# Kernel tuning notes

Measured on AMD Instinct MI355X. Metric: run time of the kernel, lower is better.

## Reference

```python
import jax, jax.numpy as jnp
import numpy as np

LORA_ALPHA = 16.0
TOP_K = 2


def setup_inputs() -> dict:
    key = jax.random.key(0)
    k_x, k_w, k_g, k_a, k_b = jax.random.split(key, 5)
    B, S, H, O, E, R = 2, 2048, 2048, 2048, 8, 16
    x = jax.random.normal(k_x, (B, S, H), dtype=jnp.float32)
    weight = jax.random.normal(k_w, (O, H), dtype=jnp.float32)          # frozen base W [out, in]
    gate_w = jax.random.normal(k_g, (E, H), dtype=jnp.float32) * 0.02   # router gate [E, in]
    A_w = jax.random.normal(k_a, (E, R, H), dtype=jnp.float32) * (1.0 / np.sqrt(H))  # stacked lora_A
    B_w = jax.random.normal(k_b, (E, O, R), dtype=jnp.float32) * 0.01   # stacked lora_B
    return {"x": x, "weight": weight, "gate_w": gate_w, "A_w": A_w, "B_w": B_w}


def reference(x, weight, gate_w, A_w, B_w):
    E = gate_w.shape[0]
    # Base frozen linear: F.linear(x, weight)
    out = jnp.einsum("bsh,oh->bso", x, weight)

    # Router: softmax over experts, top-2, renormalize
    logits = jnp.einsum("bsh,eh->bse", x, gate_w)
    probs = jax.nn.softmax(logits, axis=-1)
    topk_w, topk_idx = jax.lax.top_k(probs, TOP_K)          # [b,s,2]
    topk_w = topk_w / jnp.sum(topk_w, axis=-1, keepdims=True)

    # Per-token combine weight for each expert (sum over the 2 slots)
    onehot = jax.nn.one_hot(topk_idx, E, dtype=x.dtype)      # [b,s,2,E]
    cw = jnp.einsum("bsk,bske->bse", topk_w, onehot)         # [b,s,E]

    # LoRA: down-project into all experts' rank spaces, weight, then up-project.
    # t: [b,s,E,r] is small (r=16); weighting here avoids a [b,s,E,out] buffer.
    t = jnp.einsum("bsh,erh->bser", x, A_w)
    t = t * cw[..., None]
    lora = jnp.einsum("bser,eor->bso", t, B_w)

    return out + LORA_ALPHA * lora
```

## Files before the change

### kernel.cpp

```cpp
#include <hip/hip_runtime.h>
#include <hip/hip_bf16.h>


typedef __bf16 bf16x8 __attribute__((ext_vector_type(8)));
typedef float f32x4 __attribute__((ext_vector_type(4)));

__device__ __forceinline__ __bf16 f2bf(float f) {
  union { float f; unsigned u; } v; v.f = f;
  unsigned r = (v.u + 0x7FFFu + ((v.u >> 16) & 1u)) >> 16;
  unsigned short s = (unsigned short)r;
  return __builtin_bit_cast(__bf16, s);
}

__device__ __forceinline__ void ld_lds16(const void* g, void* l) {
  __builtin_amdgcn_global_load_lds((__attribute__((address_space(1))) void*)g,
                                   (__attribute__((address_space(3))) void*)l,
                                   16, 0, 0);
}

__global__ void conv2048(const float* __restrict__ src, __bf16* __restrict__ dst,
                         int dld) {
  const size_t r = blockIdx.x;
  const int c = threadIdx.x * 8;
  const float4* s = (const float4*)(src + r * 2048 + c);
  float4 a = s[0], b = s[1];
  bf16x8 v;
  v[0] = f2bf(a.x); v[1] = f2bf(a.y); v[2] = f2bf(a.z); v[3] = f2bf(a.w);
  v[4] = f2bf(b.x); v[5] = f2bf(b.y); v[6] = f2bf(b.z); v[7] = f2bf(b.w);
  *(bf16x8*)(dst + r * dld + c) = v;
}

__global__ void pack_bw(const float* __restrict__ Bw, __bf16* __restrict__ Bfull) {
  const int idx = blockIdx.x * 256 + threadIdx.x;
  const int e = idx >> 11, o = idx & 2047;
  const float4* s = (const float4*)(Bw + ((size_t)e * 2048 + o) * 16);
  float4 v0 = s[0], v1 = s[1], v2 = s[2], v3 = s[3];
  __bf16* d = Bfull + (size_t)o * 2176 + 2048 + e * 16;
  bf16x8 lo, hi;
  lo[0] = f2bf(v0.x); lo[1] = f2bf(v0.y); lo[2] = f2bf(v0.z); lo[3] = f2bf(v0.w);
  lo[4] = f2bf(v1.x); lo[5] = f2bf(v1.y); lo[6] = f2bf(v1.z); lo[7] = f2bf(v1.w);
  hi[0] = f2bf(v2.x); hi[1] = f2bf(v2.y); hi[2] = f2bf(v2.z); hi[3] = f2bf(v2.w);
  hi[4] = f2bf(v3.x); hi[5] = f2bf(v3.y); hi[6] = f2bf(v3.z); hi[7] = f2bf(v3.w);
  *(bf16x8*)d = lo;
  *(bf16x8*)(d + 8) = hi;
}

__global__ void router_kernel(const float* __restrict__ x, const float* __restrict__ gw,
                              __bf16* __restrict__ Abuf, float* __restrict__ cw) {
  const int t = blockIdx.x, tid = threadIdx.x;
  const float* xr = x + (size_t)t * 2048;
  const int c = tid * 8;
  float4 v0 = *(const float4*)(xr + c);
  float4 v1 = *(const float4*)(xr + c + 4);
  float xs[8] = {v0.x, v0.y, v0.z, v0.w, v1.x, v1.y, v1.z, v1.w};
  bf16x8 bv;
#pragma unroll
  for (int j = 0; j < 8; ++j) bv[j] = f2bf(xs[j]);
  *(bf16x8*)(Abuf + (size_t)t * 2176 + c) = bv;

  float acc[8] = {0, 0, 0, 0, 0, 0, 0, 0};
#pragma unroll
  for (int j = 0; j < 8; ++j) {
    const float xv = xs[j];
#pragma unroll
    for (int e = 0; e < 8; ++e) acc[e] += xv * gw[e * 2048 + c + j];
  }
#pragma unroll
  for (int e = 0; e < 8; ++e)
    for (int off = 32; off; off >>= 1) acc[e] += __shfl_down(acc[e], off);

  __shared__ float red[4][8];
  const int wave = tid >> 6, lane = tid & 63;
  if (lane == 0) {
#pragma unroll
    for (int e = 0; e < 8; ++e) red[wave][e] = acc[e];
  }
  __syncthreads();
  if (tid == 0) {
    float lg[8];
#pragma unroll
    for (int e = 0; e < 8; ++e) lg[e] = red[0][e] + red[1][e] + red[2][e] + red[3][e];
    int a = 0;
    for (int e = 1; e < 8; ++e) if (lg[e] > lg[a]) a = e;
    int b = (a == 0) ? 1 : 0;
    for (int e = 0; e < 8; ++e) if (e != a && lg[e] > lg[b]) b = e;
    const float d = __expf(lg[b] - lg[a]);
    const float wa = 1.0f / (1.0f + d), wb = d / (1.0f + d);
    float o[8] = {0, 0, 0, 0, 0, 0, 0, 0};
    o[a] = wa; o[b] = wb;
#pragma unroll
    for (int e = 0; e < 8; ++e) cw[t * 8 + e] = o[e];
  }
}

__global__ void t2_finish(const float* __restrict__ tpart, const float* __restrict__ cw,
                          __bf16* __restrict__ Abuf) {
  const int idx = blockIdx.x * 256 + threadIdx.x;
  const int t = idx >> 7, k2 = idx & 127;
  float s = tpart[idx] + tpart[idx + 524288] + tpart[idx + 2 * 524288] +
            tpart[idx + 3 * 524288];
  const float w = cw[t * 8 + (k2 >> 4)] * 16.0f;
  Abuf[(size_t)t * 2176 + 2048 + k2] = f2bf(s * w);
}

__global__ __launch_bounds__(256) void mfma_gemm_bt(
    const __bf16* __restrict__ A, const __bf16* __restrict__ B,
    float* __restrict__ C, int lda, int ldb, int ldc, int kiters,
    long long czstride) {
  __shared__ __align__(16) __bf16 As[128 * 64];
  __shared__ __align__(16) __bf16 Bs[128 * 64];
  const int tid = threadIdx.x;
  const int wave = tid >> 6;
  const int lane = tid & 63;
  const int tm = blockIdx.x * 128;
  const int tn = blockIdx.y * 128;
  C += (long long)blockIdx.z * czstride;

  const int wm = (wave >> 1) * 64;
  const int wn = (wave & 1) * 64;
  const int srow = lane >> 3;
  const int skoff = (lane & 7) * 8;

  f32x4 acc[4][4] = {};

  int kcur = blockIdx.z * kiters * 64;
  for (int kt = 0; kt < kiters; ++kt) {
#pragma unroll
    for (int r = 0; r < 4; ++r) {
      const int ch = r * 4 + wave;
      ld_lds16(A + (size_t)(tm + ch * 8 + srow) * lda + kcur + skoff, &As[ch * 512]);
      ld_lds16(B + (size_t)(tn + ch * 8 + srow) * ldb + kcur + skoff, &Bs[ch * 512]);
    }
    __syncthreads();
#pragma unroll
    for (int ks = 0; ks < 2; ++ks) {
      bf16x8 af[4], bfg[4];
#pragma unroll
      for (int i = 0; i < 4; ++i)
        af[i] = *(const bf16x8*)&As[(wm + i * 16 + (lane & 15)) * 64 + ks * 32 + (lane >> 4) * 8];
#pragma unroll
      for (int j = 0; j < 4; ++j)
        bfg[j] = *(const bf16x8*)&Bs[(wn + j * 16 + (lane & 15)) * 64 + ks * 32 + (lane >> 4) * 8];
#pragma unroll
      for (int i = 0; i < 4; ++i)
#pragma unroll
        for (int j = 0; j < 4; ++j)
          acc[i][j] = __builtin_amdgcn_mfma_f32_16x16x32_bf16(af[i], bfg[j], acc[i][j], 0, 0, 0);
    }
    __syncthreads();
    kcur += 64;
  }

  const int crow0 = tm + wm + (lane >> 4) * 4;
  const int ccol0 = tn + wn + (lane & 15);
#pragma unroll
  for (int i = 0; i < 4; ++i)
#pragma unroll
    for (int j = 0; j < 4; ++j)
#pragma unroll
      for (int rg = 0; rg < 4; ++rg)
        C[(size_t)(crow0 + i * 16 + rg) * ldc + ccol0 + j * 16] = acc[i][j][rg];
}

extern "C" void kernel_launch(void* const* d_in, const int* in_sizes, int n_in,
                              void* d_out, int out_size, void* d_ws, size_t ws_size,
                              hipStream_t stream) {
  const float* x = (const float*)d_in[0];
  const float* weight = (const float*)d_in[1];
  const float* gate_w = (const float*)d_in[2];
  const float* A_w = (const float*)d_in[3];
  const float* B_w = (const float*)d_in[4];
  float* out = (float*)d_out;

  char* ws = (char*)d_ws;
  __bf16* Abuf = (__bf16*)ws;
  __bf16* Bfull = (__bf16*)(ws + 17825792);
  __bf16* A2 = (__bf16*)(ws + 26738688);
  float* tpart = (float*)(ws + 27262976);
  float* cw = (float*)(ws + 35651584);

  conv2048<<<2048, 256, 0, stream>>>(weight, Bfull, 2176);
  conv2048<<<128, 256, 0, stream>>>(A_w, A2, 2048);
  pack_bw<<<64, 256, 0, stream>>>(B_w, Bfull);
  router_kernel<<<4096, 256, 0, stream>>>(x, gate_w, Abuf, cw);
  mfma_gemm_bt<<<dim3(32, 1, 4), 256, 0, stream>>>(Abuf, A2, tpart, 2176, 2048, 128,
                                                   8, 524288LL);
  t2_finish<<<2048, 256, 0, stream>>>(tpart, cw, Abuf);
  mfma_gemm_bt<<<dim3(32, 16, 1), 256, 0, stream>>>(Abuf, Bfull, out, 2176, 2176,
                                                    2048, 34, 0LL);
}
```

Baseline: 189.9 us.

## Swizzle GEMM LDS layout, merge prep kernels, stage gate weights in LDS

```diff
diff --git a/kernel.cpp b/kernel.cpp
--- a/kernel.cpp
+++ b/kernel.cpp
@@ -18,68 +18,83 @@
                                    16, 0, 0);
 }
 
-__global__ void conv2048(const float* __restrict__ src, __bf16* __restrict__ dst,
-                         int dld) {
-  const size_t r = blockIdx.x;
-  const int c = threadIdx.x * 8;
-  const float4* s = (const float4*)(src + r * 2048 + c);
-  float4 a = s[0], b = s[1];
-  bf16x8 v;
-  v[0] = f2bf(a.x); v[1] = f2bf(a.y); v[2] = f2bf(a.z); v[3] = f2bf(a.w);
-  v[4] = f2bf(b.x); v[5] = f2bf(b.y); v[6] = f2bf(b.z); v[7] = f2bf(b.w);
-  *(bf16x8*)(dst + r * dld + c) = v;
-}
-
-__global__ void pack_bw(const float* __restrict__ Bw, __bf16* __restrict__ Bfull) {
-  const int idx = blockIdx.x * 256 + threadIdx.x;
-  const int e = idx >> 11, o = idx & 2047;
-  const float4* s = (const float4*)(Bw + ((size_t)e * 2048 + o) * 16);
-  float4 v0 = s[0], v1 = s[1], v2 = s[2], v3 = s[3];
-  __bf16* d = Bfull + (size_t)o * 2176 + 2048 + e * 16;
-  bf16x8 lo, hi;
-  lo[0] = f2bf(v0.x); lo[1] = f2bf(v0.y); lo[2] = f2bf(v0.z); lo[3] = f2bf(v0.w);
-  lo[4] = f2bf(v1.x); lo[5] = f2bf(v1.y); lo[6] = f2bf(v1.z); lo[7] = f2bf(v1.w);
-  hi[0] = f2bf(v2.x); hi[1] = f2bf(v2.y); hi[2] = f2bf(v2.z); hi[3] = f2bf(v2.w);
-  hi[4] = f2bf(v3.x); hi[5] = f2bf(v3.y); hi[6] = f2bf(v3.z); hi[7] = f2bf(v3.w);
-  *(bf16x8*)d = lo;
-  *(bf16x8*)(d + 8) = hi;
-}
-
-__global__ void router_kernel(const float* __restrict__ x, const float* __restrict__ gw,
-                              __bf16* __restrict__ Abuf, float* __restrict__ cw) {
-  const int t = blockIdx.x, tid = threadIdx.x;
-  const float* xr = x + (size_t)t * 2048;
+__global__ void prep_kernel(const float* __restrict__ W, const float* __restrict__ Aw,
+                            const float* __restrict__ Bw, __bf16* __restrict__ Bfull,
+                            __bf16* __restrict__ A2) {
+  const int b = blockIdx.x, tid = threadIdx.x;
+  if (b < 2176) {
+    const float* src = (b < 2048) ? (W + (size_t)b * 2048)
+                                  : (Aw + (size_t)(b - 2048) * 2048);
+    __bf16* dst = (b < 2048) ? (Bfull + (size_t)b * 2176)
+                             : (A2 + (size_t)(b - 2048) * 2048);
+    const int c = tid * 8;
+    float4 a = *(const float4*)(src + c);
+    float4 d = *(const float4*)(src + c + 4);
+    bf16x8 v;
+    v[0] = f2bf(a.x); v[1] = f2bf(a.y); v[2] = f2bf(a.z); v[3] = f2bf(a.w);
+    v[4] = f2bf(d.x); v[5] = f2bf(d.y); v[6] = f2bf(d.z); v[7] = f2bf(d.w);
+    *(bf16x8*)(dst + c) = v;
+  } else {
+    const int idx = (b - 2176) * 256 + tid;
+    const int e = idx >> 11, o = idx & 2047;
+    const float4* s = (const float4*)(Bw + ((size_t)e * 2048 + o) * 16);
+    float4 v0 = s[0], v1 = s[1], v2 = s[2], v3 = s[3];
+    __bf16* d = Bfull + (size_t)o * 2176 + 2048 + e * 16;
+    bf16x8 lo, hi;
+    lo[0] = f2bf(v0.x); lo[1] = f2bf(v0.y); lo[2] = f2bf(v0.z); lo[3] = f2bf(v0.w);
+    lo[4] = f2bf(v1.x); lo[5] = f2bf(v1.y); lo[6] = f2bf(v1.z); lo[7] = f2bf(v1.w);
+    hi[0] = f2bf(v2.x); hi[1] = f2bf(v2.y); hi[2] = f2bf(v2.z); hi[3] = f2bf(v2.w);
+    hi[4] = f2bf(v3.x); hi[5] = f2bf(v3.y); hi[6] = f2bf(v3.z); hi[7] = f2bf(v3.w);
+    *(bf16x8*)d = lo;
+    *(bf16x8*)(d + 8) = hi;
+  }
+}
+
+__global__ __launch_bounds__(256) void router_kernel(
+    const float* __restrict__ x, const float* __restrict__ gw,
+    __bf16* __restrict__ Abuf, float* __restrict__ cw) {
+  __shared__ float gws[8 * 2048];
+  __shared__ float red[8][4][8];
+  const int tid = threadIdx.x;
+  const int wave = tid >> 6, lane = tid & 63;
+  for (int i = tid; i < 4096; i += 256) ((float4*)gws)[i] = ((const float4*)gw)[i];
+  __syncthreads();
+
+  const int t0 = blockIdx.x * 8;
   const int c = tid * 8;
-  float4 v0 = *(const float4*)(xr + c);
-  float4 v1 = *(const float4*)(xr + c + 4);
-  float xs[8] = {v0.x, v0.y, v0.z, v0.w, v1.x, v1.y, v1.z, v1.w};
-  bf16x8 bv;
-#pragma unroll
-  for (int j = 0; j < 8; ++j) bv[j] = f2bf(xs[j]);
-  *(bf16x8*)(Abuf + (size_t)t * 2176 + c) = bv;
-
-  float acc[8] = {0, 0, 0, 0, 0, 0, 0, 0};
-#pragma unroll
-  for (int j = 0; j < 8; ++j) {
-    const float xv = xs[j];
-#pragma unroll
-    for (int e = 0; e < 8; ++e) acc[e] += xv * gw[e * 2048 + c + j];
-  }
-#pragma unroll
-  for (int e = 0; e < 8; ++e)
-    for (int off = 32; off; off >>= 1) acc[e] += __shfl_down(acc[e], off);
-
-  __shared__ float red[4][8];
-  const int wave = tid >> 6, lane = tid & 63;
-  if (lane == 0) {
-#pragma unroll
-    for (int e = 0; e < 8; ++e) red[wave][e] = acc[e];
+  for (int tk = 0; tk < 8; ++tk) {
+    const int t = t0 + tk;
+    const float* xr = x + (size_t)t * 2048;
+    float4 v0 = *(const float4*)(xr + c);
+    float4 v1 = *(const float4*)(xr + c + 4);
+    float xs[8] = {v0.x, v0.y, v0.z, v0.w, v1.x, v1.y, v1.z, v1.w};
+    bf16x8 bv;
+#pragma unroll
+    for (int j = 0; j < 8; ++j) bv[j] = f2bf(xs[j]);
+    *(bf16x8*)(Abuf + (size_t)t * 2176 + c) = bv;
+
+    float acc[8] = {0, 0, 0, 0, 0, 0, 0, 0};
+#pragma unroll
+    for (int j = 0; j < 8; ++j) {
+      const float xv = xs[j];
+#pragma unroll
+      for (int e = 0; e < 8; ++e) acc[e] += xv * gws[e * 2048 + c + j];
+    }
+#pragma unroll
+    for (int e = 0; e < 8; ++e)
+      for (int off = 32; off; off >>= 1) acc[e] += __shfl_down(acc[e], off);
+    if (lane == 0) {
+#pragma unroll
+      for (int e = 0; e < 8; ++e) red[tk][wave][e] = acc[e];
+    }
   }
   __syncthreads();
-  if (tid == 0) {
+  if (tid < 8) {
+    const int tk = tid, t = t0 + tk;
     float lg[8];
 #pragma unroll
-    for (int e = 0; e < 8; ++e) lg[e] = red[0][e] + red[1][e] + red[2][e] + red[3][e];
+    for (int e = 0; e < 8; ++e)
+      lg[e] = red[tk][0][e] + red[tk][1][e] + red[tk][2][e] + red[tk][3][e];
     int a = 0;
     for (int e = 1; e < 8; ++e) if (lg[e] > lg[a]) a = e;
     int b = (a == 0) ? 1 : 0;
@@ -119,7 +134,11 @@
   const int wm = (wave >> 1) * 64;
   const int wn = (wave & 1) * 64;
   const int srow = lane >> 3;
-  const int skoff = (lane & 7) * 8;
+  const int skoff = ((lane & 7) ^ srow) * 8;
+
+  const int rlo = lane & 7;
+  const int rb3 = (lane >> 3) & 1;
+  const int qb = lane >> 4;
 
   f32x4 acc[4][4] = {};
 
@@ -136,11 +155,17 @@
     for (int ks = 0; ks < 2; ++ks) {
       bf16x8 af[4], bfg[4];
 #pragma unroll
-      for (int i = 0; i < 4; ++i)
-        af[i] = *(const bf16x8*)&As[(wm + i * 16 + (lane & 15)) * 64 + ks * 32 + (lane >> 4) * 8];
-#pragma unroll
-      for (int j = 0; j < 4; ++j)
-        bfg[j] = *(const bf16x8*)&Bs[(wn + j * 16 + (lane & 15)) * 64 + ks * 32 + (lane >> 4) * 8];
+      for (int i = 0; i < 4; ++i) {
+        const int rh = ((wm + i * 16) >> 3) + rb3;
+        const int q = (ks * 4 + qb) ^ rlo;
+        af[i] = *(const bf16x8*)&As[rh * 512 + rlo * 64 + q * 8];
+      }
+#pragma unroll
+      for (int j = 0; j < 4; ++j) {
+        const int rh = ((wn + j * 16) >> 3) + rb3;
+        const int q = (ks * 4 + qb) ^ rlo;
+        bfg[j] = *(const bf16x8*)&Bs[rh * 512 + rlo * 64 + q * 8];
+      }
 #pragma unroll
       for (int i = 0; i < 4; ++i)
 #pragma unroll
@@ -179,10 +204,8 @@
   float* tpart = (float*)(ws + 27262976);
   float* cw = (float*)(ws + 35651584);
 
-  conv2048<<<2048, 256, 0, stream>>>(weight, Bfull, 2176);
-  conv2048<<<128, 256, 0, stream>>>(A_w, A2, 2048);
-  pack_bw<<<64, 256, 0, stream>>>(B_w, Bfull);
-  router_kernel<<<4096, 256, 0, stream>>>(x, gate_w, Abuf, cw);
+  prep_kernel<<<2240, 256, 0, stream>>>(weight, A_w, B_w, Bfull, A2);
+  router_kernel<<<512, 256, 0, stream>>>(x, gate_w, Abuf, cw);
   mfma_gemm_bt<<<dim3(32, 1, 4), 256, 0, stream>>>(Abuf, A2, tpart, 2176, 2048, 128,
                                                    8, 524288LL);
   t2_finish<<<2048, 256, 0, stream>>>(tpart, cw, Abuf);
```

Result: faster. 174.5 us (-8.1%).
